# Performance work log

Hardware: AMD Instinct MI355X
Metric: run time of the kernel (lower is better)

Reference implementation:

```python
import jax, jax.numpy as jnp
import numpy as np

N = 10000      # nodes
E = 160000     # edges
IN = 512       # in_feat
H = 512        # hidden_dim
L = 6          # layers
C = 64         # num_class
EPS = 1e-5     # BatchNorm eps


def setup_inputs() -> dict:
    key = jax.random.key(0)
    ks = jax.random.split(key, 12)
    x = jax.random.normal(ks[0], (N, IN), jnp.float32)
    src = jax.random.randint(ks[1], (E,), 0, N)
    dst = jax.random.randint(ks[2], (E,), 0, N)
    W0 = jax.random.normal(ks[3], (IN, H), jnp.float32) * (1.0 / np.sqrt(IN))
    Ws = jax.random.normal(ks[4], (L - 1, H, H), jnp.float32) * (1.0 / np.sqrt(H))
    bs = jnp.zeros((L, H), jnp.float32)
    gamma = jnp.ones((L, H), jnp.float32) + 0.1 * jax.random.normal(ks[5], (L, H), jnp.float32)
    beta = 0.1 * jax.random.normal(ks[6], (L, H), jnp.float32)
    run_mean = 0.1 * jax.random.normal(ks[7], (L, H), jnp.float32)
    run_var = jax.random.uniform(ks[8], (L, H), jnp.float32, 0.5, 1.5)
    linW = jax.random.normal(ks[9], (L * H, C), jnp.float32) * (1.0 / np.sqrt(L * H))
    linb = jnp.zeros((C,), jnp.float32)
    return {"x": x, "W0": W0, "Ws": Ws, "bs": bs, "gamma": gamma, "beta": beta,
            "run_mean": run_mean, "run_var": run_var, "linW": linW, "linb": linb,
            "src": src, "dst": dst}


def reference(x, W0, Ws, bs, gamma, beta, run_mean, run_var, linW, linb, src, dst):
    ones_e = jnp.ones((E,), jnp.float32)
    out_deg = jax.ops.segment_sum(ones_e, src, num_segments=N)
    in_deg = jax.ops.segment_sum(ones_e, dst, num_segments=N)
    # DGL GraphConv norm='both': D_dst^{-1/2} A D_src^{-1/2}, zero-deg clamped to 1
    norm_src = jnp.clip(out_deg, 1.0, None) ** -0.5   # [N]
    norm_dst = jnp.clip(in_deg, 1.0, None) ** -0.5    # [N]

    h = x
    hs = []
    for i in range(L):
        W = W0 if i == 0 else Ws[i - 1]
        m = (h * norm_src[:, None]) @ W                 # [N, H] GEMM
        agg = jax.ops.segment_sum(m[src], dst, num_segments=N)  # gather/scatter
        h = agg * norm_dst[:, None] + bs[i]
        # BatchNorm1d (inference, running stats) + ReLU; dropout is identity in eval
        scale = gamma[i] * jax.lax.rsqrt(run_var[i] + EPS)
        h = jax.nn.relu((h - run_mean[i]) * scale + beta[i])
        hs.append(h)
    h = jnp.concatenate(hs, axis=-1)                    # [N, L*H] JK-concat
    return h @ linW + linb                              # [N, C]
```

## Files before the change

### kernel.cpp

```cpp
#include <hip/hip_runtime.h>

#define NN 10000
#define NNPAD 10112
#define NE 160000
#define HF 512
#define LL 6
#define NC 64
#define KCAT (LL*HF)
#define BN_EPS 1e-5f

typedef _Float16 f16x8 __attribute__((ext_vector_type(8)));
typedef _Float16 f16x4 __attribute__((ext_vector_type(4)));
typedef float f32x4 __attribute__((ext_vector_type(4)));

#define GLB(p) ((const __attribute__((address_space(1))) void*)(p))
#define LDSP(p) ((__attribute__((address_space(3))) void*)(p))


__global__ void zero_u32_kernel(unsigned* __restrict__ p, int n) {
  int i = blockIdx.x * blockDim.x + threadIdx.x;
  if (i < n) p[i] = 0u;
}

__global__ void deg_kernel(const int* __restrict__ src, const int* __restrict__ dst,
                           unsigned* __restrict__ cnt_out, unsigned* __restrict__ cnt_in) {
  int e = blockIdx.x * blockDim.x + threadIdx.x;
  if (e < NE) {
    atomicAdd(&cnt_out[src[e]], 1u);
    atomicAdd(&cnt_in[dst[e]], 1u);
  }
}

__global__ void norm_kernel(const unsigned* __restrict__ cnt_out, const unsigned* __restrict__ cnt_in,
                            float* __restrict__ norm_src, float* __restrict__ norm_dst) {
  int i = blockIdx.x * blockDim.x + threadIdx.x;
  if (i < NN) {
    unsigned co = cnt_out[i]; if (co < 1u) co = 1u;
    unsigned ci = cnt_in[i];  if (ci < 1u) ci = 1u;
    norm_src[i] = rsqrtf((float)co);
    norm_dst[i] = rsqrtf((float)ci);
  }
}

__global__ void bn_prep(const float* __restrict__ bs, const float* __restrict__ gamma,
                        const float* __restrict__ beta, const float* __restrict__ rmean,
                        const float* __restrict__ rvar,
                        float* __restrict__ scale, float* __restrict__ shift) {
  int i = blockIdx.x * blockDim.x + threadIdx.x;
  if (i < LL * HF) {
    float s = gamma[i] * rsqrtf(rvar[i] + BN_EPS);
    scale[i] = s;
    shift[i] = (bs[i] - rmean[i]) * s + beta[i];
  }
}

__global__ void scan_kernel(const unsigned* __restrict__ cnt, unsigned* __restrict__ off) {
  __shared__ unsigned wsum[16];
  int tid = threadIdx.x;
  int lane = tid & 63, wid = tid >> 6;
  unsigned base = 0;
  for (int c = 0; c < NN; c += 1024) {
    int i = c + tid;
    unsigned v = (i < NN) ? cnt[i] : 0u;
    unsigned x = v;
    #pragma unroll
    for (int d = 1; d < 64; d <<= 1) {
      unsigned y = __shfl_up(x, d, 64);
      if (lane >= d) x += y;
    }
    if (lane == 63) wsum[wid] = x;
    __syncthreads();
    if (wid == 0 && lane < 16) {
      unsigned s = wsum[lane];
      #pragma unroll
      for (int d = 1; d < 16; d <<= 1) {
        unsigned y = __shfl_up(s, d, 16);
        if (lane >= d) s += y;
      }
      wsum[lane] = s;
    }
    __syncthreads();
    unsigned wbase = wid ? wsum[wid - 1] : 0u;
    if (i < NN) off[i] = base + wbase + x - v;
    unsigned tot = wsum[15];
    __syncthreads();
    base += tot;
  }
  if (tid == 0) off[NN] = base;
}

__global__ void fill_kernel(const int* __restrict__ src, const int* __restrict__ dst,
                            const unsigned* __restrict__ off, unsigned* __restrict__ cursor,
                            int* __restrict__ edge_src) {
  int e = blockIdx.x * blockDim.x + threadIdx.x;
  if (e < NE) {
    int d = dst[e];
    unsigned p = atomicAdd(&cursor[d], 1u);
    edge_src[off[d] + p] = src[e];
  }
}

__global__ void convert_w(const float* __restrict__ W0, const float* __restrict__ Ws,
                          _Float16* __restrict__ Wt) {
  int l = blockIdx.z;
  const float* W = (l == 0) ? W0 : (Ws + (size_t)(l - 1) * HF * HF);
  __shared__ float t[32][33];
  int n0 = blockIdx.x * 32, k0 = blockIdx.y * 32;
  int tx = threadIdx.x & 31, ty4 = (threadIdx.x >> 5) * 4;
  #pragma unroll
  for (int j = 0; j < 4; ++j)
    t[ty4 + j][tx] = W[(size_t)(k0 + ty4 + j) * HF + n0 + tx];
  __syncthreads();
  size_t base = (size_t)l * HF * HF;
  #pragma unroll
  for (int j = 0; j < 4; ++j)
    Wt[base + (size_t)(n0 + ty4 + j) * HF + k0 + tx] = (_Float16)t[tx][ty4 + j];
}

__global__ void convert_lin(const float* __restrict__ linW, _Float16* __restrict__ Lt) {
  __shared__ float t[32][33];
  int n0 = blockIdx.x * 32, k0 = blockIdx.y * 32;
  int tx = threadIdx.x & 31, ty4 = (threadIdx.x >> 5) * 4;
  #pragma unroll
  for (int j = 0; j < 4; ++j)
    t[ty4 + j][tx] = linW[(size_t)(k0 + ty4 + j) * NC + n0 + tx];
  __syncthreads();
  #pragma unroll
  for (int j = 0; j < 4; ++j)
    Lt[(size_t)(n0 + ty4 + j) * KCAT + k0 + tx] = (_Float16)t[tx][ty4 + j];
}

__global__ void split_x(const float* __restrict__ x, const float* __restrict__ nsrc,
                        _Float16* __restrict__ zh) {
  int i = blockIdx.x * blockDim.x + threadIdx.x;
  if (i >= NN * HF / 4) return;
  int base = i * 4;
  int row = base >> 9;
  float ns = nsrc[row];
  float4 v = *(const float4*)&x[base];
  f16x4 h;
  h.x = (_Float16)(v.x * ns);
  h.y = (_Float16)(v.y * ns);
  h.z = (_Float16)(v.z * ns);
  h.w = (_Float16)(v.w * ns);
  *(f16x4*)&zh[base] = h;
}

__launch_bounds__(256, 2)
__global__ void gemm_layer_f16(const _Float16* __restrict__ Z,
                               const _Float16* __restrict__ Wt,
                               _Float16* __restrict__ Mout) {
  __shared__ _Float16 As[2][128][64];
  __shared__ _Float16 Bs[2][128][64];
  int m0 = blockIdx.y * 128;
  int n0 = blockIdx.x * 128;
  int wid = threadIdx.x >> 6, lane = threadIdx.x & 63;
  int wr = wid >> 1, wc = wid & 1;
  int fr = lane & 15, kg = lane >> 4;
  int rr = lane >> 3;
  int ck = (lane & 7) ^ rr;

  f32x4 acc[4][4];
  #pragma unroll
  for (int m = 0; m < 4; ++m)
    #pragma unroll
    for (int n = 0; n < 4; ++n)
      acc[m][n] = (f32x4){0.f, 0.f, 0.f, 0.f};

  const _Float16* gA = Z  + (size_t)(m0 + wid * 32 + rr) * HF + ck * 8;
  const _Float16* gB = Wt + (size_t)(n0 + wid * 32 + rr) * HF + ck * 8;

  auto stage = [&](int buf, int k0) {
    #pragma unroll
    for (int i = 0; i < 4; ++i) {
      __builtin_amdgcn_global_load_lds(GLB(gA + (size_t)i * 8 * HF + k0),
                                       LDSP(&As[buf][wid * 32 + i * 8][0]), 16, 0, 0);
      __builtin_amdgcn_global_load_lds(GLB(gB + (size_t)i * 8 * HF + k0),
                                       LDSP(&Bs[buf][wid * 32 + i * 8][0]), 16, 0, 0);
    }
  };

  stage(0, 0);
  __syncthreads();
  int cur = 0;
  for (int t = 0; t < HF / 64; ++t) {
    if (t < HF / 64 - 1) stage(cur ^ 1, (t + 1) * 64);
    #pragma unroll
    for (int kk = 0; kk < 2; ++kk) {
      f16x8 a[4], b[4];
      #pragma unroll
      for (int n = 0; n < 4; ++n) {
        int row = wc * 64 + n * 16 + fr;
        b[n] = *(const f16x8*)&Bs[cur][row][((kk * 4 + kg) ^ (row & 7)) * 8];
      }
      #pragma unroll
      for (int m = 0; m < 4; ++m) {
        int row = wr * 64 + m * 16 + fr;
        a[m] = *(const f16x8*)&As[cur][row][((kk * 4 + kg) ^ (row & 7)) * 8];
      }
      #pragma unroll
      for (int m = 0; m < 4; ++m)
        #pragma unroll
        for (int n = 0; n < 4; ++n)
          acc[m][n] = __builtin_amdgcn_mfma_f32_16x16x32_f16(a[m], b[n], acc[m][n], 0, 0, 0);
    }
    __syncthreads();
    cur ^= 1;
  }
  #pragma unroll
  for (int m = 0; m < 4; ++m) {
    #pragma unroll
    for (int j = 0; j < 4; ++j) {
      int row = m0 + wr * 64 + m * 16 + kg * 4 + j;
      if (row < NN) {
        #pragma unroll
        for (int n = 0; n < 4; ++n) {
          int col = n0 + wc * 64 + n * 16 + fr;
          Mout[(size_t)row * HF + col] = (_Float16)acc[m][n][j];
        }
      }
    }
  }
}

__launch_bounds__(256)
__global__ void agg_bn_kernel(const _Float16* __restrict__ Mm,
                              const int* __restrict__ edge_src,
                              const unsigned* __restrict__ row_off,
                              const float* __restrict__ norm_dst,
                              const float* __restrict__ norm_src,
                              const float* __restrict__ bn_scale,
                              const float* __restrict__ bn_shift,
                              _Float16* __restrict__ hcat_col,
                              _Float16* __restrict__ zh) {
  int n = blockIdx.x * 4 + (threadIdx.x >> 6);
  if (n >= NN) return;
  int f = (threadIdx.x & 63) * 8;
  unsigned e0 = row_off[n], e1 = row_off[n + 1];
  float a0=0.f,a1=0.f,a2=0.f,a3=0.f,a4=0.f,a5=0.f,a6=0.f,a7=0.f;
  unsigned e = e0;
  for (; e + 4 <= e1; e += 4) {
    int s0 = edge_src[e], s1 = edge_src[e + 1], s2 = edge_src[e + 2], s3 = edge_src[e + 3];
    f16x8 v0 = *(const f16x8*)&Mm[(size_t)s0 * HF + f];
    f16x8 v1 = *(const f16x8*)&Mm[(size_t)s1 * HF + f];
    f16x8 v2 = *(const f16x8*)&Mm[(size_t)s2 * HF + f];
    f16x8 v3 = *(const f16x8*)&Mm[(size_t)s3 * HF + f];
    a0 += (float)v0[0]+(float)v1[0]+(float)v2[0]+(float)v3[0];
    a1 += (float)v0[1]+(float)v1[1]+(float)v2[1]+(float)v3[1];
    a2 += (float)v0[2]+(float)v1[2]+(float)v2[2]+(float)v3[2];
    a3 += (float)v0[3]+(float)v1[3]+(float)v2[3]+(float)v3[3];
    a4 += (float)v0[4]+(float)v1[4]+(float)v2[4]+(float)v3[4];
    a5 += (float)v0[5]+(float)v1[5]+(float)v2[5]+(float)v3[5];
    a6 += (float)v0[6]+(float)v1[6]+(float)v2[6]+(float)v3[6];
    a7 += (float)v0[7]+(float)v1[7]+(float)v2[7]+(float)v3[7];
  }
  for (; e < e1; ++e) {
    int s = edge_src[e];
    f16x8 v = *(const f16x8*)&Mm[(size_t)s * HF + f];
    a0 += (float)v[0]; a1 += (float)v[1]; a2 += (float)v[2]; a3 += (float)v[3];
    a4 += (float)v[4]; a5 += (float)v[5]; a6 += (float)v[6]; a7 += (float)v[7];
  }
  float nd = norm_dst[n];
  float4 s0 = *(const float4*)&bn_scale[f];
  float4 s1 = *(const float4*)&bn_scale[f + 4];
  float4 t0 = *(const float4*)&bn_shift[f];
  float4 t1 = *(const float4*)&bn_shift[f + 4];
  float y0 = fmaxf(fmaf(a0 * nd, s0.x, t0.x), 0.f);
  float y1 = fmaxf(fmaf(a1 * nd, s0.y, t0.y), 0.f);
  float y2 = fmaxf(fmaf(a2 * nd, s0.z, t0.z), 0.f);
  float y3 = fmaxf(fmaf(a3 * nd, s0.w, t0.w), 0.f);
  float y4 = fmaxf(fmaf(a4 * nd, s1.x, t1.x), 0.f);
  float y5 = fmaxf(fmaf(a5 * nd, s1.y, t1.y), 0.f);
  float y6 = fmaxf(fmaf(a6 * nd, s1.z, t1.z), 0.f);
  float y7 = fmaxf(fmaf(a7 * nd, s1.w, t1.w), 0.f);
  f16x8 hv;
  hv[0]=(_Float16)y0; hv[1]=(_Float16)y1; hv[2]=(_Float16)y2; hv[3]=(_Float16)y3;
  hv[4]=(_Float16)y4; hv[5]=(_Float16)y5; hv[6]=(_Float16)y6; hv[7]=(_Float16)y7;
  *(f16x8*)&hcat_col[(size_t)n * KCAT + f] = hv;
  if (zh) {
    float ns = norm_src[n];
    f16x8 zv;
    zv[0]=(_Float16)(y0*ns); zv[1]=(_Float16)(y1*ns); zv[2]=(_Float16)(y2*ns); zv[3]=(_Float16)(y3*ns);
    zv[4]=(_Float16)(y4*ns); zv[5]=(_Float16)(y5*ns); zv[6]=(_Float16)(y6*ns); zv[7]=(_Float16)(y7*ns);
    *(f16x8*)&zh[(size_t)n * HF + f] = zv;
  }
}

__launch_bounds__(256, 2)
__global__ void final_gemm_f16(const _Float16* __restrict__ Hc,
                               const _Float16* __restrict__ Lt,
                               float* __restrict__ part) {
  __shared__ _Float16 As[2][128][64];
  __shared__ _Float16 Bs[2][64][64];
  int m0 = blockIdx.x * 128;
  int sp = blockIdx.y;
  int kbase = sp * HF;
  int wid = threadIdx.x >> 6, lane = threadIdx.x & 63;
  int fr = lane & 15, kg = lane >> 4;
  int rr = lane >> 3;
  int ck = (lane & 7) ^ rr;

  f32x4 acc[2][4];
  #pragma unroll
  for (int m = 0; m < 2; ++m)
    #pragma unroll
    for (int n = 0; n < 4; ++n)
      acc[m][n] = (f32x4){0.f, 0.f, 0.f, 0.f};

  const _Float16* gA = Hc + (size_t)(m0 + wid * 32 + rr) * KCAT + kbase + ck * 8;
  const _Float16* gB = Lt + (size_t)(wid * 16 + rr) * KCAT + kbase + ck * 8;

  auto stage = [&](int buf, int k0) {
    #pragma unroll
    for (int i = 0; i < 4; ++i)
      __builtin_amdgcn_global_load_lds(GLB(gA + (size_t)i * 8 * KCAT + k0),
                                       LDSP(&As[buf][wid * 32 + i * 8][0]), 16, 0, 0);
    #pragma unroll
    for (int i = 0; i < 2; ++i)
      __builtin_amdgcn_global_load_lds(GLB(gB + (size_t)i * 8 * KCAT + k0),
                                       LDSP(&Bs[buf][wid * 16 + i * 8][0]), 16, 0, 0);
  };

  stage(0, 0);
  __syncthreads();
  int cur = 0;
  for (int t = 0; t < HF / 64; ++t) {
    if (t < HF / 64 - 1) stage(cur ^ 1, (t + 1) * 64);
    #pragma unroll
    for (int kk = 0; kk < 2; ++kk) {
      f16x8 a[2], b[4];
      #pragma unroll
      for (int n = 0; n < 4; ++n) {
        int row = n * 16 + fr;
        b[n] = *(const f16x8*)&Bs[cur][row][((kk * 4 + kg) ^ (row & 7)) * 8];
      }
      #pragma unroll
      for (int m = 0; m < 2; ++m) {
        int row = wid * 32 + m * 16 + fr;
        a[m] = *(const f16x8*)&As[cur][row][((kk * 4 + kg) ^ (row & 7)) * 8];
      }
      #pragma unroll
      for (int m = 0; m < 2; ++m)
        #pragma unroll
        for (int n = 0; n < 4; ++n)
          acc[m][n] = __builtin_amdgcn_mfma_f32_16x16x32_f16(a[m], b[n], acc[m][n], 0, 0, 0);
    }
    __syncthreads();
    cur ^= 1;
  }
  #pragma unroll
  for (int m = 0; m < 2; ++m) {
    #pragma unroll
    for (int j = 0; j < 4; ++j) {
      int row = m0 + wid * 32 + m * 16 + kg * 4 + j;
      if (row < NN) {
        #pragma unroll
        for (int n = 0; n < 4; ++n) {
          int col = n * 16 + fr;
          part[((size_t)sp * NN + row) * NC + col] = acc[m][n][j];
        }
      }
    }
  }
}

__launch_bounds__(256)
__global__ void final_reduce(const float* __restrict__ part,
                             const float* __restrict__ linb,
                             float* __restrict__ out) {
  int i = blockIdx.x * blockDim.x + threadIdx.x;
  if (i >= NN * NC / 4) return;
  int n  = i >> 4;
  int cq = i & 15;
  float4 s = *(const float4*)&linb[cq * 4];
  #pragma unroll
  for (int sp = 0; sp < LL; ++sp) {
    float4 v = *(const float4*)&part[((size_t)sp * NN + n) * NC + cq * 4];
    s.x += v.x; s.y += v.y; s.z += v.z; s.w += v.w;
  }
  *(float4*)&out[(size_t)n * NC + cq * 4] = s;
}


extern "C" void kernel_launch(void* const* d_in, const int* in_sizes, int n_in,
                              void* d_out, int out_size, void* d_ws, size_t ws_size,
                              hipStream_t stream) {
  const float* x     = (const float*)d_in[0];
  const float* W0    = (const float*)d_in[1];
  const float* Ws    = (const float*)d_in[2];
  const float* bs    = (const float*)d_in[3];
  const float* gamma = (const float*)d_in[4];
  const float* beta  = (const float*)d_in[5];
  const float* rmean = (const float*)d_in[6];
  const float* rvar  = (const float*)d_in[7];
  const float* linW  = (const float*)d_in[8];
  const float* linb  = (const float*)d_in[9];
  const int*   src   = (const int*)d_in[10];
  const int*   dst   = (const int*)d_in[11];
  float* out = (float*)d_out;

  char* w = (char*)d_ws;
  size_t o = 0;
  auto carve = [&](size_t bytes) -> void* {
    o = (o + 255) & ~(size_t)255;
    void* p = w + o;
    o += bytes;
    return p;
  };
  _Float16*  m_buf = (_Float16*)carve((size_t)NNPAD * HF * 2);
  _Float16*  hcat  = (_Float16*)carve((size_t)NNPAD * KCAT * 2);
  _Float16*  zh    = (_Float16*)carve((size_t)NNPAD * HF * 2);
  _Float16*  wt    = (_Float16*)carve((size_t)LL * HF * HF * 2);
  _Float16*  lt    = (_Float16*)carve((size_t)NC * KCAT * 2);
  float*     part  = (float*)carve((size_t)LL * NN * NC * 4);
  float*     bnsc  = (float*)carve((size_t)LL * HF * 4);
  float*     bnsh  = (float*)carve((size_t)LL * HF * 4);
  float*     nsrc  = (float*)carve((size_t)NN * 4);
  float*     ndst  = (float*)carve((size_t)NN * 4);
  unsigned*  cnts  = (unsigned*)carve((size_t)3 * NN * 4);
  unsigned*  roff  = (unsigned*)carve((size_t)(NN + 1) * 4);
  int*       esrc  = (int*)carve((size_t)NE * 4);

  unsigned* cnt_out = cnts;
  unsigned* cnt_in  = cnts + NN;
  unsigned* cursor  = cnts + 2 * NN;

  zero_u32_kernel<<<(3 * NN + 255) / 256, 256, 0, stream>>>(cnts, 3 * NN);
  deg_kernel<<<(NE + 255) / 256, 256, 0, stream>>>(src, dst, cnt_out, cnt_in);
  norm_kernel<<<(NN + 255) / 256, 256, 0, stream>>>(cnt_out, cnt_in, nsrc, ndst);
  bn_prep<<<(LL * HF + 255) / 256, 256, 0, stream>>>(bs, gamma, beta, rmean, rvar, bnsc, bnsh);
  scan_kernel<<<1, 1024, 0, stream>>>(cnt_in, roff);
  fill_kernel<<<(NE + 255) / 256, 256, 0, stream>>>(src, dst, roff, cursor, esrc);
  convert_w<<<dim3(16, 16, 6), 256, 0, stream>>>(W0, Ws, wt);
  convert_lin<<<dim3(2, 96), 256, 0, stream>>>(linW, lt);
  split_x<<<(NN * HF / 4 + 255) / 256, 256, 0, stream>>>(x, nsrc, zh);

  for (int l = 0; l < LL; ++l) {
    gemm_layer_f16<<<dim3(HF / 128, NNPAD / 128), 256, 0, stream>>>(
        zh, wt + (size_t)l * HF * HF, m_buf);
    bool last = (l == LL - 1);
    agg_bn_kernel<<<(NN + 3) / 4, 256, 0, stream>>>(m_buf, esrc, roff, ndst, nsrc,
                                                    bnsc + l * HF, bnsh + l * HF,
                                                    hcat + (size_t)l * HF,
                                                    last ? nullptr : zh);
  }
  final_gemm_f16<<<dim3(NNPAD / 128, LL), 256, 0, stream>>>(hcat, lt, part);
  final_reduce<<<(NN * NC / 4 + 255) / 256, 256, 0, stream>>>(part, linb, out);
}
```

Measured before the change: 306.0 us.

## Apply source norm in aggregation, read layer input from hcat, single-buffer GEMMs

The source-degree normalisation moves out of the GEMM input and into the aggregation, where each gathered row is scaled by norm_src of its source. The layer GEMM can then read the previous layer's output straight from the JK-concat buffer with a stride argument, so the extra zh write in agg_bn is dropped. Both GEMMs switch from double-buffered LDS staging to a single buffer with two barriers per k-step, which halves LDS use but removes the load/compute overlap. The two small prep kernels are merged into one launch, and the aggregation now does an extra scalar gather per edge.

```diff
diff --git a/kernel.cpp b/kernel.cpp
--- a/kernel.cpp
+++ b/kernel.cpp
@@ -31,8 +31,12 @@
   }
 }
 
-__global__ void norm_kernel(const unsigned* __restrict__ cnt_out, const unsigned* __restrict__ cnt_in,
-                            float* __restrict__ norm_src, float* __restrict__ norm_dst) {
+__global__ void prep_kernel(const unsigned* __restrict__ cnt_out, const unsigned* __restrict__ cnt_in,
+                            float* __restrict__ norm_src, float* __restrict__ norm_dst,
+                            const float* __restrict__ bs, const float* __restrict__ gamma,
+                            const float* __restrict__ beta, const float* __restrict__ rmean,
+                            const float* __restrict__ rvar,
+                            float* __restrict__ scale, float* __restrict__ shift) {
   int i = blockIdx.x * blockDim.x + threadIdx.x;
   if (i < NN) {
     unsigned co = cnt_out[i]; if (co < 1u) co = 1u;
@@ -40,13 +44,6 @@
     norm_src[i] = rsqrtf((float)co);
     norm_dst[i] = rsqrtf((float)ci);
   }
-}
-
-__global__ void bn_prep(const float* __restrict__ bs, const float* __restrict__ gamma,
-                        const float* __restrict__ beta, const float* __restrict__ rmean,
-                        const float* __restrict__ rvar,
-                        float* __restrict__ scale, float* __restrict__ shift) {
-  int i = blockIdx.x * blockDim.x + threadIdx.x;
   if (i < LL * HF) {
     float s = gamma[i] * rsqrtf(rvar[i] + BN_EPS);
     scale[i] = s;
@@ -130,28 +127,25 @@
     Lt[(size_t)(n0 + ty4 + j) * KCAT + k0 + tx] = (_Float16)t[tx][ty4 + j];
 }
 
-__global__ void split_x(const float* __restrict__ x, const float* __restrict__ nsrc,
-                        _Float16* __restrict__ zh) {
+__global__ void split_x(const float* __restrict__ x, _Float16* __restrict__ zh) {
   int i = blockIdx.x * blockDim.x + threadIdx.x;
   if (i >= NN * HF / 4) return;
   int base = i * 4;
-  int row = base >> 9;
-  float ns = nsrc[row];
   float4 v = *(const float4*)&x[base];
   f16x4 h;
-  h.x = (_Float16)(v.x * ns);
-  h.y = (_Float16)(v.y * ns);
-  h.z = (_Float16)(v.z * ns);
-  h.w = (_Float16)(v.w * ns);
+  h.x = (_Float16)v.x;
+  h.y = (_Float16)v.y;
+  h.z = (_Float16)v.z;
+  h.w = (_Float16)v.w;
   *(f16x4*)&zh[base] = h;
 }
 
 __launch_bounds__(256, 2)
-__global__ void gemm_layer_f16(const _Float16* __restrict__ Z,
+__global__ void gemm_layer_f16(const _Float16* __restrict__ Z, int lda,
                                const _Float16* __restrict__ Wt,
                                _Float16* __restrict__ Mout) {
-  __shared__ _Float16 As[2][128][64];
-  __shared__ _Float16 Bs[2][128][64];
+  __shared__ _Float16 As[128][64];
+  __shared__ _Float16 Bs[128][64];
   int m0 = blockIdx.y * 128;
   int n0 = blockIdx.x * 128;
   int wid = threadIdx.x >> 6, lane = threadIdx.x & 63;
@@ -167,36 +161,31 @@
     for (int n = 0; n < 4; ++n)
       acc[m][n] = (f32x4){0.f, 0.f, 0.f, 0.f};
 
-  const _Float16* gA = Z  + (size_t)(m0 + wid * 32 + rr) * HF + ck * 8;
+  const _Float16* gA = Z  + (size_t)(m0 + wid * 32 + rr) * lda + ck * 8;
   const _Float16* gB = Wt + (size_t)(n0 + wid * 32 + rr) * HF + ck * 8;
 
-  auto stage = [&](int buf, int k0) {
+  for (int k0 = 0; k0 < HF; k0 += 64) {
+    __syncthreads();
     #pragma unroll
     for (int i = 0; i < 4; ++i) {
-      __builtin_amdgcn_global_load_lds(GLB(gA + (size_t)i * 8 * HF + k0),
-                                       LDSP(&As[buf][wid * 32 + i * 8][0]), 16, 0, 0);
+      __builtin_amdgcn_global_load_lds(GLB(gA + (size_t)i * 8 * lda + k0),
+                                       LDSP(&As[wid * 32 + i * 8][0]), 16, 0, 0);
       __builtin_amdgcn_global_load_lds(GLB(gB + (size_t)i * 8 * HF + k0),
-                                       LDSP(&Bs[buf][wid * 32 + i * 8][0]), 16, 0, 0);
-    }
-  };
-
-  stage(0, 0);
-  __syncthreads();
-  int cur = 0;
-  for (int t = 0; t < HF / 64; ++t) {
-    if (t < HF / 64 - 1) stage(cur ^ 1, (t + 1) * 64);
+                                       LDSP(&Bs[wid * 32 + i * 8][0]), 16, 0, 0);
+    }
+    __syncthreads();
     #pragma unroll
     for (int kk = 0; kk < 2; ++kk) {
       f16x8 a[4], b[4];
       #pragma unroll
       for (int n = 0; n < 4; ++n) {
         int row = wc * 64 + n * 16 + fr;
-        b[n] = *(const f16x8*)&Bs[cur][row][((kk * 4 + kg) ^ (row & 7)) * 8];
+        b[n] = *(const f16x8*)&Bs[row][((kk * 4 + kg) ^ (row & 7)) * 8];
       }
       #pragma unroll
       for (int m = 0; m < 4; ++m) {
         int row = wr * 64 + m * 16 + fr;
-        a[m] = *(const f16x8*)&As[cur][row][((kk * 4 + kg) ^ (row & 7)) * 8];
+        a[m] = *(const f16x8*)&As[row][((kk * 4 + kg) ^ (row & 7)) * 8];
       }
       #pragma unroll
       for (int m = 0; m < 4; ++m)
@@ -204,8 +193,6 @@
         for (int n = 0; n < 4; ++n)
           acc[m][n] = __builtin_amdgcn_mfma_f32_16x16x32_f16(a[m], b[n], acc[m][n], 0, 0, 0);
     }
-    __syncthreads();
-    cur ^= 1;
   }
   #pragma unroll
   for (int m = 0; m < 4; ++m) {
@@ -231,8 +218,7 @@
                               const float* __restrict__ norm_src,
                               const float* __restrict__ bn_scale,
                               const float* __restrict__ bn_shift,
-                              _Float16* __restrict__ hcat_col,
-                              _Float16* __restrict__ zh) {
+                              _Float16* __restrict__ hcat_col) {
   int n = blockIdx.x * 4 + (threadIdx.x >> 6);
   if (n >= NN) return;
   int f = (threadIdx.x & 63) * 8;
@@ -241,24 +227,28 @@
   unsigned e = e0;
   for (; e + 4 <= e1; e += 4) {
     int s0 = edge_src[e], s1 = edge_src[e + 1], s2 = edge_src[e + 2], s3 = edge_src[e + 3];
+    float n0 = norm_src[s0], n1 = norm_src[s1], n2 = norm_src[s2], n3 = norm_src[s3];
     f16x8 v0 = *(const f16x8*)&Mm[(size_t)s0 * HF + f];
     f16x8 v1 = *(const f16x8*)&Mm[(size_t)s1 * HF + f];
     f16x8 v2 = *(const f16x8*)&Mm[(size_t)s2 * HF + f];
     f16x8 v3 = *(const f16x8*)&Mm[(size_t)s3 * HF + f];
-    a0 += (float)v0[0]+(float)v1[0]+(float)v2[0]+(float)v3[0];
-    a1 += (float)v0[1]+(float)v1[1]+(float)v2[1]+(float)v3[1];
-    a2 += (float)v0[2]+(float)v1[2]+(float)v2[2]+(float)v3[2];
-    a3 += (float)v0[3]+(float)v1[3]+(float)v2[3]+(float)v3[3];
-    a4 += (float)v0[4]+(float)v1[4]+(float)v2[4]+(float)v3[4];
-    a5 += (float)v0[5]+(float)v1[5]+(float)v2[5]+(float)v3[5];
-    a6 += (float)v0[6]+(float)v1[6]+(float)v2[6]+(float)v3[6];
-    a7 += (float)v0[7]+(float)v1[7]+(float)v2[7]+(float)v3[7];
+    a0 = fmaf((float)v0[0], n0, fmaf((float)v1[0], n1, fmaf((float)v2[0], n2, fmaf((float)v3[0], n3, a0))));
+    a1 = fmaf((float)v0[1], n0, fmaf((float)v1[1], n1, fmaf((float)v2[1], n2, fmaf((float)v3[1], n3, a1))));
+    a2 = fmaf((float)v0[2], n0, fmaf((float)v1[2], n1, fmaf((float)v2[2], n2, fmaf((float)v3[2], n3, a2))));
+    a3 = fmaf((float)v0[3], n0, fmaf((float)v1[3], n1, fmaf((float)v2[3], n2, fmaf((float)v3[3], n3, a3))));
+    a4 = fmaf((float)v0[4], n0, fmaf((float)v1[4], n1, fmaf((float)v2[4], n2, fmaf((float)v3[4], n3, a4))));
+    a5 = fmaf((float)v0[5], n0, fmaf((float)v1[5], n1, fmaf((float)v2[5], n2, fmaf((float)v3[5], n3, a5))));
+    a6 = fmaf((float)v0[6], n0, fmaf((float)v1[6], n1, fmaf((float)v2[6], n2, fmaf((float)v3[6], n3, a6))));
+    a7 = fmaf((float)v0[7], n0, fmaf((float)v1[7], n1, fmaf((float)v2[7], n2, fmaf((float)v3[7], n3, a7))));
   }
   for (; e < e1; ++e) {
     int s = edge_src[e];
+    float ns = norm_src[s];
     f16x8 v = *(const f16x8*)&Mm[(size_t)s * HF + f];
-    a0 += (float)v[0]; a1 += (float)v[1]; a2 += (float)v[2]; a3 += (float)v[3];
-    a4 += (float)v[4]; a5 += (float)v[5]; a6 += (float)v[6]; a7 += (float)v[7];
+    a0 = fmaf((float)v[0], ns, a0); a1 = fmaf((float)v[1], ns, a1);
+    a2 = fmaf((float)v[2], ns, a2); a3 = fmaf((float)v[3], ns, a3);
+    a4 = fmaf((float)v[4], ns, a4); a5 = fmaf((float)v[5], ns, a5);
+    a6 = fmaf((float)v[6], ns, a6); a7 = fmaf((float)v[7], ns, a7);
   }
   float nd = norm_dst[n];
   float4 s0 = *(const float4*)&bn_scale[f];
@@ -277,21 +267,14 @@
   hv[0]=(_Float16)y0; hv[1]=(_Float16)y1; hv[2]=(_Float16)y2; hv[3]=(_Float16)y3;
   hv[4]=(_Float16)y4; hv[5]=(_Float16)y5; hv[6]=(_Float16)y6; hv[7]=(_Float16)y7;
   *(f16x8*)&hcat_col[(size_t)n * KCAT + f] = hv;
-  if (zh) {
-    float ns = norm_src[n];
-    f16x8 zv;
-    zv[0]=(_Float16)(y0*ns); zv[1]=(_Float16)(y1*ns); zv[2]=(_Float16)(y2*ns); zv[3]=(_Float16)(y3*ns);
-    zv[4]=(_Float16)(y4*ns); zv[5]=(_Float16)(y5*ns); zv[6]=(_Float16)(y6*ns); zv[7]=(_Float16)(y7*ns);
-    *(f16x8*)&zh[(size_t)n * HF + f] = zv;
-  }
 }
 
 __launch_bounds__(256, 2)
 __global__ void final_gemm_f16(const _Float16* __restrict__ Hc,
                                const _Float16* __restrict__ Lt,
                                float* __restrict__ part) {
-  __shared__ _Float16 As[2][128][64];
-  __shared__ _Float16 Bs[2][64][64];
+  __shared__ _Float16 As[128][64];
+  __shared__ _Float16 Bs[64][64];
   int m0 = blockIdx.x * 128;
   int sp = blockIdx.y;
   int kbase = sp * HF;
@@ -310,34 +293,29 @@
   const _Float16* gA = Hc + (size_t)(m0 + wid * 32 + rr) * KCAT + kbase + ck * 8;
   const _Float16* gB = Lt + (size_t)(wid * 16 + rr) * KCAT + kbase + ck * 8;
 
-  auto stage = [&](int buf, int k0) {
+  for (int k0 = 0; k0 < HF; k0 += 64) {
+    __syncthreads();
     #pragma unroll
     for (int i = 0; i < 4; ++i)
       __builtin_amdgcn_global_load_lds(GLB(gA + (size_t)i * 8 * KCAT + k0),
-                                       LDSP(&As[buf][wid * 32 + i * 8][0]), 16, 0, 0);
+                                       LDSP(&As[wid * 32 + i * 8][0]), 16, 0, 0);
     #pragma unroll
     for (int i = 0; i < 2; ++i)
       __builtin_amdgcn_global_load_lds(GLB(gB + (size_t)i * 8 * KCAT + k0),
-                                       LDSP(&Bs[buf][wid * 16 + i * 8][0]), 16, 0, 0);
-  };
-
-  stage(0, 0);
-  __syncthreads();
-  int cur = 0;
-  for (int t = 0; t < HF / 64; ++t) {
-    if (t < HF / 64 - 1) stage(cur ^ 1, (t + 1) * 64);
+                                       LDSP(&Bs[wid * 16 + i * 8][0]), 16, 0, 0);
+    __syncthreads();
     #pragma unroll
     for (int kk = 0; kk < 2; ++kk) {
       f16x8 a[2], b[4];
       #pragma unroll
       for (int n = 0; n < 4; ++n) {
         int row = n * 16 + fr;
-        b[n] = *(const f16x8*)&Bs[cur][row][((kk * 4 + kg) ^ (row & 7)) * 8];
+        b[n] = *(const f16x8*)&Bs[row][((kk * 4 + kg) ^ (row & 7)) * 8];
       }
       #pragma unroll
       for (int m = 0; m < 2; ++m) {
         int row = wid * 32 + m * 16 + fr;
-        a[m] = *(const f16x8*)&As[cur][row][((kk * 4 + kg) ^ (row & 7)) * 8];
+        a[m] = *(const f16x8*)&As[row][((kk * 4 + kg) ^ (row & 7)) * 8];
       }
       #pragma unroll
       for (int m = 0; m < 2; ++m)
@@ -345,8 +323,6 @@
         for (int n = 0; n < 4; ++n)
           acc[m][n] = __builtin_amdgcn_mfma_f32_16x16x32_f16(a[m], b[n], acc[m][n], 0, 0, 0);
     }
-    __syncthreads();
-    cur ^= 1;
   }
   #pragma unroll
   for (int m = 0; m < 2; ++m) {
@@ -427,22 +403,22 @@
 
   zero_u32_kernel<<<(3 * NN + 255) / 256, 256, 0, stream>>>(cnts, 3 * NN);
   deg_kernel<<<(NE + 255) / 256, 256, 0, stream>>>(src, dst, cnt_out, cnt_in);
-  norm_kernel<<<(NN + 255) / 256, 256, 0, stream>>>(cnt_out, cnt_in, nsrc, ndst);
-  bn_prep<<<(LL * HF + 255) / 256, 256, 0, stream>>>(bs, gamma, beta, rmean, rvar, bnsc, bnsh);
+  prep_kernel<<<(NN + 255) / 256, 256, 0, stream>>>(cnt_out, cnt_in, nsrc, ndst,
+                                                    bs, gamma, beta, rmean, rvar, bnsc, bnsh);
   scan_kernel<<<1, 1024, 0, stream>>>(cnt_in, roff);
   fill_kernel<<<(NE + 255) / 256, 256, 0, stream>>>(src, dst, roff, cursor, esrc);
   convert_w<<<dim3(16, 16, 6), 256, 0, stream>>>(W0, Ws, wt);
   convert_lin<<<dim3(2, 96), 256, 0, stream>>>(linW, lt);
-  split_x<<<(NN * HF / 4 + 255) / 256, 256, 0, stream>>>(x, nsrc, zh);
+  split_x<<<(NN * HF / 4 + 255) / 256, 256, 0, stream>>>(x, zh);
 
   for (int l = 0; l < LL; ++l) {
+    const _Float16* A   = (l == 0) ? zh : (hcat + (size_t)(l - 1) * HF);
+    int             lda = (l == 0) ? HF : KCAT;
     gemm_layer_f16<<<dim3(HF / 128, NNPAD / 128), 256, 0, stream>>>(
-        zh, wt + (size_t)l * HF * HF, m_buf);
-    bool last = (l == LL - 1);
+        A, lda, wt + (size_t)l * HF * HF, m_buf);
     agg_bn_kernel<<<(NN + 3) / 4, 256, 0, stream>>>(m_buf, esrc, roff, ndst, nsrc,
                                                     bnsc + l * HF, bnsh + l * HF,
-                                                    hcat + (size_t)l * HF,
-                                                    last ? nullptr : zh);
+                                                    hcat + (size_t)l * HF);
   }
   final_gemm_f16<<<dim3(NNPAD / 128, LL), 256, 0, stream>>>(hcat, lt, part);
   final_reduce<<<(NN * NC / 4 + 255) / 256, 256, 0, stream>>>(part, linb, out);
```

Result: faster. 285.0 us (-6.9%).
